# Optimization experiments

Measured on AMD Instinct MI355X. Metric: run time of the kernel, lower is better.

The kernel has to match this reference:

```python
import jax, jax.numpy as jnp
import numpy as np


def setup_inputs() -> dict:
    key = jax.random.key(0)
    ks = jax.random.split(key, 6)
    B, F, C = 2048, 512, 64
    t_feat = jax.random.normal(ks[0], (B, F), dtype=jnp.float32)
    f_feat = jax.random.normal(ks[1], (B, F), dtype=jnp.float32)
    # proj Linear(F*F -> C); scale like torch default init (~1/sqrt(fan_in))
    W_proj = jax.random.normal(ks[2], (C, F * F), dtype=jnp.float32) / np.sqrt(F * F)
    b_proj = jnp.zeros((C,), dtype=jnp.float32)
    W1 = jax.random.normal(ks[3], (32, C), dtype=jnp.float32) / np.sqrt(C)
    b1 = jnp.zeros((32,), dtype=jnp.float32)
    W2 = jax.random.normal(ks[4], (1, 32), dtype=jnp.float32) / np.sqrt(32)
    b2 = jnp.zeros((1,), dtype=jnp.float32)
    return {"t_feat": t_feat, "f_feat": f_feat, "W_proj": W_proj, "b_proj": b_proj,
            "W1": W1, "b1": b1, "W2": W2, "b2": b2}


def reference(t_feat, f_feat, W_proj, b_proj, W1, b1, W2, b2):
    B, F = t_feat.shape
    C = W_proj.shape[0]
    # corr[b,i,j] = t[b,i] * f[b,j]; proj = corr_flat @ W_proj.T + b_proj.
    # Equivalent bilinear form computed WITHOUT materializing the (B,F,F) outer product:
    Wr = W_proj.reshape(C, F, F)            # W_proj[c, i*F + j] -> Wr[c,i,j]
    tmp = jnp.einsum('bi,cij->bcj', t_feat, Wr)   # (B, C, F)
    proj = jnp.einsum('bcj,bj->bc', tmp, f_feat) + b_proj  # (B, C)
    h = jax.nn.relu(proj)
    # GRL is identity in forward
    h2 = jax.nn.relu(h @ W1.T + b1)          # (B, 32)
    logit = h2 @ W2.T + b2                   # (B, 1)
    return logit
```

## Files before the change

kernel.cpp:

```cpp
#include <hip/hip_runtime.h>
#include <hip/hip_bf16.h>
#include <stdint.h>

#define BATCH 2048
#define FDIM 512
#define CDIM 64

typedef unsigned short ushort_t;
typedef __attribute__((ext_vector_type(8))) short short8;
typedef __attribute__((ext_vector_type(4))) float f32x4;

__device__ __forceinline__ ushort_t f2bf(float x) {
    union { float f; uint32_t u; } v; v.f = x;
    uint32_t u = v.u;
    uint32_t r = u + 0x7FFFu + ((u >> 16) & 1u);
    return (ushort_t)(r >> 16);
}
__device__ __forceinline__ float bf2f(ushort_t u) {
    union { float f; uint32_t v; } x; x.v = ((uint32_t)u) << 16; return x.f;
}

__global__ void convert_kernel(const float* __restrict__ src, ushort_t* __restrict__ dst) {
    int idx = blockIdx.x * 256 + threadIdx.x;
    float4 v0 = ((const float4*)src)[idx * 2];
    float4 v1 = ((const float4*)src)[idx * 2 + 1];
    ushort_t p[8] = { f2bf(v0.x), f2bf(v0.y), f2bf(v0.z), f2bf(v0.w),
                      f2bf(v1.x), f2bf(v1.y), f2bf(v1.z), f2bf(v1.w) };
    *(uint4*)&dst[idx * 8] = *(uint4*)p;
}

__global__ void convert_ft_kernel(const float* __restrict__ f, ushort_t* __restrict__ f16,
                                  const float* __restrict__ t, ushort_t* __restrict__ t16) {
    int blk = blockIdx.x;
    const float* src = (blk < 512) ? f : t;
    ushort_t* dst    = (blk < 512) ? f16 : t16;
    int idx = (blk & 511) * 256 + threadIdx.x;
    float4 v0 = ((const float4*)src)[idx * 2];
    float4 v1 = ((const float4*)src)[idx * 2 + 1];
    ushort_t p[8] = { f2bf(v0.x), f2bf(v0.y), f2bf(v0.z), f2bf(v0.w),
                      f2bf(v1.x), f2bf(v1.y), f2bf(v1.z), f2bf(v1.w) };
    *(uint4*)&dst[idx * 8] = *(uint4*)p;
}

#define AS3(p) ((__attribute__((address_space(3))) void*)(p))
#define AS1(p) ((const __attribute__((address_space(1))) void*)(p))

__launch_bounds__(256, 2)
__global__ void gemm_fused_kernel(const ushort_t* __restrict__ f16,
                                  const ushort_t* __restrict__ Wb,
                                  const ushort_t* __restrict__ t16,
                                  float* __restrict__ part) {
    __shared__ ushort_t As[128 * 32];
    __shared__ ushort_t Bs[128 * 32];
    __shared__ float scratch[256];

    const int tid  = threadIdx.x;
    const int wave = tid >> 6;
    const int lane = tid & 63;
    const int l15  = lane & 15;
    const int lg   = lane >> 4;

    const int b0 = blockIdx.x * 128;
    const int n0 = blockIdx.y * 128;

    const int m_base = (wave >> 1) * 64;
    const int nh     = wave & 1;
    const int n_base = nh * 64;

    f32x4 acc[4][4];
    #pragma unroll
    for (int mi = 0; mi < 4; mi++)
        #pragma unroll
        for (int ni = 0; ni < 4; ni++)
            acc[mi][ni] = (f32x4){0.f, 0.f, 0.f, 0.f};

    const int p    = tid >> 2;
    const int cph  = tid & 3;
    const int cg   = cph ^ ((p >> 1) & 3);
    const int nrot = ((p & 15) << 2) | (p >> 4);

    const ushort_t* gA0 = f16 + (size_t)(b0 + p) * FDIM + cg * 8;
    const ushort_t* gA1 = f16 + (size_t)(b0 + 64 + p) * FDIM + cg * 8;
    const ushort_t* gB0 = Wb + (size_t)(n0 + nrot) * FDIM + cg * 8;
    const ushort_t* gB1 = Wb + (size_t)(n0 + 64 + nrot) * FDIM + cg * 8;

    for (int k0 = 0; k0 < FDIM; k0 += 32) {
        __builtin_amdgcn_global_load_lds(AS1(gA0 + k0), AS3(&As[0 * 2048 + wave * 512]), 16, 0, 0);
        __builtin_amdgcn_global_load_lds(AS1(gA1 + k0), AS3(&As[1 * 2048 + wave * 512]), 16, 0, 0);
        __builtin_amdgcn_global_load_lds(AS1(gB0 + k0), AS3(&Bs[0 * 2048 + wave * 512]), 16, 0, 0);
        __builtin_amdgcn_global_load_lds(AS1(gB1 + k0), AS3(&Bs[1 * 2048 + wave * 512]), 16, 0, 0);
        __syncthreads();

        short8 a[4], b[4];
        #pragma unroll
        for (int mi = 0; mi < 4; mi++) {
            int r = m_base + mi * 16 + l15;
            a[mi] = *(const short8*)&As[r * 32 + (lg ^ ((r >> 1) & 3)) * 8];
        }
        #pragma unroll
        for (int ni = 0; ni < 4; ni++) {
            int q = n_base + ni * 16 + l15;
            b[ni] = *(const short8*)&Bs[q * 32 + (lg ^ ((q >> 1) & 3)) * 8];
        }

        #pragma unroll
        for (int mi = 0; mi < 4; mi++)
            #pragma unroll
            for (int ni = 0; ni < 4; ni++)
                acc[mi][ni] = __builtin_amdgcn_mfma_f32_16x16x32_bf16(a[mi], b[ni], acc[mi][ni], 0, 0, 0);

        __syncthreads();
    }

    const int c  = n0 >> 9;
    const int iq = (n0 >> 7) & 3;
    const int i_base = (n0 & 511) + n_base + l15 * 4;

    #pragma unroll
    for (int mi = 0; mi < 4; mi++) {
        #pragma unroll
        for (int r = 0; r < 4; r++) {
            int b_idx = b0 + m_base + mi * 16 + lg * 4 + r;
            ushort4 tv = *(const ushort4*)&t16[(size_t)b_idx * FDIM + i_base];
            float sv = acc[mi][0][r] * bf2f(tv.x) + acc[mi][1][r] * bf2f(tv.y)
                     + acc[mi][2][r] * bf2f(tv.z) + acc[mi][3][r] * bf2f(tv.w);
            sv += __shfl_xor(sv, 1, 64);
            sv += __shfl_xor(sv, 2, 64);
            sv += __shfl_xor(sv, 4, 64);
            sv += __shfl_xor(sv, 8, 64);
            if (l15 == 0)
                scratch[(m_base + mi * 16 + lg * 4 + r) * 2 + nh] = sv;
        }
    }
    __syncthreads();
    if (tid < 128) {
        float v = scratch[tid * 2] + scratch[tid * 2 + 1];
        part[(((size_t)(b0 + tid)) * 64 + c) * 4 + iq] = v;
    }
}

__global__ void mlp_kernel(const float* __restrict__ part,
                           const float* __restrict__ b_proj,
                           const float* __restrict__ W1, const float* __restrict__ b1,
                           const float* __restrict__ W2, const float* __restrict__ b2,
                           float* __restrict__ out) {
    __shared__ float h[8][64];
    const int tid = threadIdx.x;
    const int bl  = tid >> 5;
    const int o   = tid & 31;
    const int b   = blockIdx.x * 8 + bl;

    #pragma unroll
    for (int c = o; c < 64; c += 32) {
        float4 v = *(const float4*)&part[(((size_t)b * 64 + c)) * 4];
        float sv = v.x + v.y + v.z + v.w + b_proj[c];
        h[bl][c] = sv > 0.f ? sv : 0.f;
    }
    __syncthreads();

    float sv = b1[o];
    #pragma unroll
    for (int c = 0; c < 64; c++) sv += h[bl][c] * W1[o * 64 + c];
    float v = (sv > 0.f ? sv : 0.f) * W2[o];
    v += __shfl_xor(v, 1, 32);
    v += __shfl_xor(v, 2, 32);
    v += __shfl_xor(v, 4, 32);
    v += __shfl_xor(v, 8, 32);
    v += __shfl_xor(v, 16, 32);
    if (o == 0) out[b] = v + b2[0];
}

extern "C" void kernel_launch(void* const* d_in, const int* in_sizes, int n_in,
                              void* d_out, int out_size, void* d_ws, size_t ws_size,
                              hipStream_t stream) {
    const float* t_feat = (const float*)d_in[0];
    const float* f_feat = (const float*)d_in[1];
    const float* W_proj = (const float*)d_in[2];
    const float* b_proj = (const float*)d_in[3];
    const float* W1     = (const float*)d_in[4];
    const float* b1     = (const float*)d_in[5];
    const float* W2     = (const float*)d_in[6];
    const float* b2     = (const float*)d_in[7];
    float* out = (float*)d_out;

    uint8_t* ws = (uint8_t*)d_ws;
    ushort_t* Wb   = (ushort_t*)(ws);
    ushort_t* f16  = (ushort_t*)(ws + 33554432);
    ushort_t* t16  = (ushort_t*)(ws + 33554432 + 2097152);
    float*    part = (float*)(ws + 33554432 + 2 * 2097152);

    convert_kernel<<<dim3((CDIM * FDIM * FDIM) / 2048), dim3(256), 0, stream>>>(W_proj, Wb);
    convert_ft_kernel<<<dim3(1024), dim3(256), 0, stream>>>(f_feat, f16, t_feat, t16);

    gemm_fused_kernel<<<dim3(BATCH / 128, (CDIM * FDIM) / 128), dim3(256), 0, stream>>>(
        f16, Wb, t16, part);

    mlp_kernel<<<dim3(BATCH / 8), dim3(256), 0, stream>>>(part, b_proj, W1, b1, W2, b2, out);
}
```

Measured before the change: 213.9 us.

## Merge conversion kernels and fuse MLP tail into GEMM via last-block counter

The three bf16 conversion passes are merged into one prep kernel, which also zeroes a per-row-tile atomic counter. The separate MLP kernel is folded into the GEMM: each block increments a counter after writing its partials, and the last of the 256 column blocks for a row tile runs the bias, ReLU and two small linear layers for those 128 rows. This removes two kernel launches and their gaps. In exchange it adds threadfences and atomics, and the tail is serialised onto one block per row tile, with a per-thread 64-element array that may raise register pressure.

```diff
diff --git a/kernel.cpp b/kernel.cpp
--- a/kernel.cpp
+++ b/kernel.cpp
@@ -20,8 +20,19 @@
     union { float f; uint32_t v; } x; x.v = ((uint32_t)u) << 16; return x.f;
 }
 
-__global__ void convert_kernel(const float* __restrict__ src, ushort_t* __restrict__ dst) {
-    int idx = blockIdx.x * 256 + threadIdx.x;
+#define WCH ((CDIM * FDIM * FDIM) / 8)
+#define FCH ((BATCH * FDIM) / 8)
+
+__global__ void prep_kernel(const float* __restrict__ W, ushort_t* __restrict__ Wb,
+                            const float* __restrict__ f, ushort_t* __restrict__ f16,
+                            const float* __restrict__ t, ushort_t* __restrict__ t16,
+                            unsigned int* __restrict__ cnt) {
+    if (blockIdx.x == 0 && threadIdx.x < 16) cnt[threadIdx.x] = 0;
+    int gid = blockIdx.x * 256 + threadIdx.x;
+    const float* src; ushort_t* dst; int idx;
+    if (gid < WCH)            { src = W; dst = Wb;  idx = gid; }
+    else if (gid < WCH + FCH) { src = f; dst = f16; idx = gid - WCH; }
+    else                      { src = t; dst = t16; idx = gid - WCH - FCH; }
     float4 v0 = ((const float4*)src)[idx * 2];
     float4 v1 = ((const float4*)src)[idx * 2 + 1];
     ushort_t p[8] = { f2bf(v0.x), f2bf(v0.y), f2bf(v0.z), f2bf(v0.w),
@@ -29,19 +40,6 @@
     *(uint4*)&dst[idx * 8] = *(uint4*)p;
 }
 
-__global__ void convert_ft_kernel(const float* __restrict__ f, ushort_t* __restrict__ f16,
-                                  const float* __restrict__ t, ushort_t* __restrict__ t16) {
-    int blk = blockIdx.x;
-    const float* src = (blk < 512) ? f : t;
-    ushort_t* dst    = (blk < 512) ? f16 : t16;
-    int idx = (blk & 511) * 256 + threadIdx.x;
-    float4 v0 = ((const float4*)src)[idx * 2];
-    float4 v1 = ((const float4*)src)[idx * 2 + 1];
-    ushort_t p[8] = { f2bf(v0.x), f2bf(v0.y), f2bf(v0.z), f2bf(v0.w),
-                      f2bf(v1.x), f2bf(v1.y), f2bf(v1.z), f2bf(v1.w) };
-    *(uint4*)&dst[idx * 8] = *(uint4*)p;
-}
-
 #define AS3(p) ((__attribute__((address_space(3))) void*)(p))
 #define AS1(p) ((const __attribute__((address_space(1))) void*)(p))
 
@@ -49,10 +47,18 @@
 __global__ void gemm_fused_kernel(const ushort_t* __restrict__ f16,
                                   const ushort_t* __restrict__ Wb,
                                   const ushort_t* __restrict__ t16,
-                                  float* __restrict__ part) {
+                                  float* __restrict__ part,
+                                  unsigned int* __restrict__ cnt,
+                                  const float* __restrict__ b_proj,
+                                  const float* __restrict__ W1,
+                                  const float* __restrict__ b1,
+                                  const float* __restrict__ W2,
+                                  const float* __restrict__ b2,
+                                  float* __restrict__ out) {
     __shared__ ushort_t As[128 * 32];
     __shared__ ushort_t Bs[128 * 32];
     __shared__ float scratch[256];
+    __shared__ int is_last;
 
     const int tid  = threadIdx.x;
     const int wave = tid >> 6;
@@ -137,37 +143,35 @@
         float v = scratch[tid * 2] + scratch[tid * 2 + 1];
         part[(((size_t)(b0 + tid)) * 64 + c) * 4 + iq] = v;
     }
-}
-
-__global__ void mlp_kernel(const float* __restrict__ part,
-                           const float* __restrict__ b_proj,
-                           const float* __restrict__ W1, const float* __restrict__ b1,
-                           const float* __restrict__ W2, const float* __restrict__ b2,
-                           float* __restrict__ out) {
-    __shared__ float h[8][64];
-    const int tid = threadIdx.x;
-    const int bl  = tid >> 5;
-    const int o   = tid & 31;
-    const int b   = blockIdx.x * 8 + bl;
-
-    #pragma unroll
-    for (int c = o; c < 64; c += 32) {
-        float4 v = *(const float4*)&part[(((size_t)b * 64 + c)) * 4];
-        float sv = v.x + v.y + v.z + v.w + b_proj[c];
-        h[bl][c] = sv > 0.f ? sv : 0.f;
+
+    __threadfence();
+    if (tid == 0) {
+        unsigned int old = atomicAdd(&cnt[blockIdx.x], 1u);
+        is_last = (old == 255u);
     }
     __syncthreads();
-
-    float sv = b1[o];
-    #pragma unroll
-    for (int c = 0; c < 64; c++) sv += h[bl][c] * W1[o * 64 + c];
-    float v = (sv > 0.f ? sv : 0.f) * W2[o];
-    v += __shfl_xor(v, 1, 32);
-    v += __shfl_xor(v, 2, 32);
-    v += __shfl_xor(v, 4, 32);
-    v += __shfl_xor(v, 8, 32);
-    v += __shfl_xor(v, 16, 32);
-    if (o == 0) out[b] = v + b2[0];
+    if (is_last) {
+        __threadfence();
+        if (tid < 128) {
+            int row = b0 + tid;
+            const float4* p4 = (const float4*)&part[(size_t)row * 256];
+            float h[64];
+            #pragma unroll
+            for (int cc = 0; cc < 64; cc++) {
+                float4 v = p4[cc];
+                float sv = v.x + v.y + v.z + v.w + b_proj[cc];
+                h[cc] = sv > 0.f ? sv : 0.f;
+            }
+            float logit = b2[0];
+            for (int o = 0; o < 32; o++) {
+                float sv = b1[o];
+                #pragma unroll
+                for (int cc = 0; cc < 64; cc++) sv += h[cc] * W1[o * 64 + cc];
+                logit += (sv > 0.f ? sv : 0.f) * W2[o];
+            }
+            out[row] = logit;
+        }
+    }
 }
 
 extern "C" void kernel_launch(void* const* d_in, const int* in_sizes, int n_in,
@@ -186,14 +190,13 @@
     uint8_t* ws = (uint8_t*)d_ws;
     ushort_t* Wb   = (ushort_t*)(ws);
     ushort_t* f16  = (ushort_t*)(ws + 33554432);
-    ushort_t* t16  = (ushort_t*)(ws + 33554432 + 2097152);
-    float*    part = (float*)(ws + 33554432 + 2 * 2097152);
-
-    convert_kernel<<<dim3((CDIM * FDIM * FDIM) / 2048), dim3(256), 0, stream>>>(W_proj, Wb);
-    convert_ft_kernel<<<dim3(1024), dim3(256), 0, stream>>>(f_feat, f16, t_feat, t16);
+    ushort_t* t16  = (ushort_t*)(ws + 35651584);
+    float*    part = (float*)(ws + 37748736);
+    unsigned int* cnt = (unsigned int*)(ws + 39845888);
+
+    prep_kernel<<<dim3(WCH / 256 + (2 * FCH) / 256), dim3(256), 0, stream>>>(
+        W_proj, Wb, f_feat, f16, t_feat, t16, cnt);
 
     gemm_fused_kernel<<<dim3(BATCH / 128, (CDIM * FDIM) / 128), dim3(256), 0, stream>>>(
-        f16, Wb, t16, part);
-
-    mlp_kernel<<<dim3(BATCH / 8), dim3(256), 0, stream>>>(part, b_proj, W1, b1, W2, b2, out);
-}
+        f16, Wb, t16, part, cnt, b_proj, W1, b1, W2, b2, out);
+}
```

Result: slower. 673.7 us (+214.9%).

## Fuse W_proj bf16 conversion into GEMM B loads, drop separate convert pass

Applied to the files above, without the earlier changes.

Drops the standalone kernel that converted the 64x512x512 fp32 W_proj to bf16 in workspace. The GEMM now loads fp32 W rows straight into registers and converts them to bf16 in-kernel, without LDS staging for B. Blocks use a 1D grid that groups the 16 batch tiles sharing one W tile onto adjacent block ids, and launch bounds rise to 4 blocks per CU. This avoids writing and re-reading a 32MB intermediate, but W is now fetched as fp32 and reconverted by each of the 16 batch blocks, relying on L2 to absorb the reuse.

```diff
diff --git a/kernel.cpp b/kernel.cpp
--- a/kernel.cpp
+++ b/kernel.cpp
@@ -20,21 +20,14 @@
     union { float f; uint32_t v; } x; x.v = ((uint32_t)u) << 16; return x.f;
 }
 
-__global__ void convert_kernel(const float* __restrict__ src, ushort_t* __restrict__ dst) {
-    int idx = blockIdx.x * 256 + threadIdx.x;
-    float4 v0 = ((const float4*)src)[idx * 2];
-    float4 v1 = ((const float4*)src)[idx * 2 + 1];
-    ushort_t p[8] = { f2bf(v0.x), f2bf(v0.y), f2bf(v0.z), f2bf(v0.w),
-                      f2bf(v1.x), f2bf(v1.y), f2bf(v1.z), f2bf(v1.w) };
-    *(uint4*)&dst[idx * 8] = *(uint4*)p;
-}
+#define FCH ((BATCH * FDIM) / 8)
 
-__global__ void convert_ft_kernel(const float* __restrict__ f, ushort_t* __restrict__ f16,
-                                  const float* __restrict__ t, ushort_t* __restrict__ t16) {
-    int blk = blockIdx.x;
-    const float* src = (blk < 512) ? f : t;
-    ushort_t* dst    = (blk < 512) ? f16 : t16;
-    int idx = (blk & 511) * 256 + threadIdx.x;
+__global__ void prep_kernel(const float* __restrict__ f, ushort_t* __restrict__ f16,
+                            const float* __restrict__ t, ushort_t* __restrict__ t16) {
+    int gid = blockIdx.x * 256 + threadIdx.x;
+    const float* src = (gid < FCH) ? f : t;
+    ushort_t* dst    = (gid < FCH) ? f16 : t16;
+    int idx = gid & (FCH - 1);
     float4 v0 = ((const float4*)src)[idx * 2];
     float4 v1 = ((const float4*)src)[idx * 2 + 1];
     ushort_t p[8] = { f2bf(v0.x), f2bf(v0.y), f2bf(v0.z), f2bf(v0.w),
@@ -45,13 +38,12 @@
 #define AS3(p) ((__attribute__((address_space(3))) void*)(p))
 #define AS1(p) ((const __attribute__((address_space(1))) void*)(p))
 
-__launch_bounds__(256, 2)
+__launch_bounds__(256, 4)
 __global__ void gemm_fused_kernel(const ushort_t* __restrict__ f16,
-                                  const ushort_t* __restrict__ Wb,
+                                  const float* __restrict__ W,
                                   const ushort_t* __restrict__ t16,
                                   float* __restrict__ part) {
     __shared__ ushort_t As[128 * 32];
-    __shared__ ushort_t Bs[128 * 32];
     __shared__ float scratch[256];
 
     const int tid  = threadIdx.x;
@@ -60,8 +52,10 @@
     const int l15  = lane & 15;
     const int lg   = lane >> 4;
 
-    const int b0 = blockIdx.x * 128;
-    const int n0 = blockIdx.y * 128;
+    const int g  = blockIdx.x;
+    const int s  = g >> 3;
+    const int b0 = (s & 15) << 7;
+    const int n0 = (((g & 7) << 5) + (s >> 4)) << 7;
 
     const int m_base = (wave >> 1) * 64;
     const int nh     = wave & 1;
@@ -74,33 +68,38 @@
         for (int ni = 0; ni < 4; ni++)
             acc[mi][ni] = (f32x4){0.f, 0.f, 0.f, 0.f};
 
-    const int p    = tid >> 2;
-    const int cph  = tid & 3;
-    const int cg   = cph ^ ((p >> 1) & 3);
-    const int nrot = ((p & 15) << 2) | (p >> 4);
-
+    const int p   = tid >> 2;
+    const int cph = tid & 3;
+    const int cg  = cph ^ ((p >> 1) & 3);
     const ushort_t* gA0 = f16 + (size_t)(b0 + p) * FDIM + cg * 8;
     const ushort_t* gA1 = f16 + (size_t)(b0 + 64 + p) * FDIM + cg * 8;
-    const ushort_t* gB0 = Wb + (size_t)(n0 + nrot) * FDIM + cg * 8;
-    const ushort_t* gB1 = Wb + (size_t)(n0 + 64 + nrot) * FDIM + cg * 8;
+
+    const float* gB = W + (size_t)(n0 + n_base + l15 * 4) * FDIM + lg * 8;
 
     for (int k0 = 0; k0 < FDIM; k0 += 32) {
+        short8 b[4];
+        #pragma unroll
+        for (int ni = 0; ni < 4; ni++) {
+            const float* bp = gB + (size_t)ni * FDIM + k0;
+            float4 v0 = *(const float4*)bp;
+            float4 v1 = *(const float4*)(bp + 4);
+            union { __hip_bfloat162 h2[4]; short8 s8; } pk;
+            pk.h2[0] = __float22bfloat162_rn(make_float2(v0.x, v0.y));
+            pk.h2[1] = __float22bfloat162_rn(make_float2(v0.z, v0.w));
+            pk.h2[2] = __float22bfloat162_rn(make_float2(v1.x, v1.y));
+            pk.h2[3] = __float22bfloat162_rn(make_float2(v1.z, v1.w));
+            b[ni] = pk.s8;
+        }
+
         __builtin_amdgcn_global_load_lds(AS1(gA0 + k0), AS3(&As[0 * 2048 + wave * 512]), 16, 0, 0);
         __builtin_amdgcn_global_load_lds(AS1(gA1 + k0), AS3(&As[1 * 2048 + wave * 512]), 16, 0, 0);
-        __builtin_amdgcn_global_load_lds(AS1(gB0 + k0), AS3(&Bs[0 * 2048 + wave * 512]), 16, 0, 0);
-        __builtin_amdgcn_global_load_lds(AS1(gB1 + k0), AS3(&Bs[1 * 2048 + wave * 512]), 16, 0, 0);
         __syncthreads();
 
-        short8 a[4], b[4];
+        short8 a[4];
         #pragma unroll
         for (int mi = 0; mi < 4; mi++) {
             int r = m_base + mi * 16 + l15;
             a[mi] = *(const short8*)&As[r * 32 + (lg ^ ((r >> 1) & 3)) * 8];
-        }
-        #pragma unroll
-        for (int ni = 0; ni < 4; ni++) {
-            int q = n_base + ni * 16 + l15;
-            b[ni] = *(const short8*)&Bs[q * 32 + (lg ^ ((q >> 1) & 3)) * 8];
         }
 
         #pragma unroll
@@ -184,16 +183,13 @@
     float* out = (float*)d_out;
 
     uint8_t* ws = (uint8_t*)d_ws;
-    ushort_t* Wb   = (ushort_t*)(ws);
-    ushort_t* f16  = (ushort_t*)(ws + 33554432);
-    ushort_t* t16  = (ushort_t*)(ws + 33554432 + 2097152);
-    float*    part = (float*)(ws + 33554432 + 2 * 2097152);
+    ushort_t* f16  = (ushort_t*)(ws);
+    ushort_t* t16  = (ushort_t*)(ws + 2097152);
+    float*    part = (float*)(ws + 4194304);
 
-    convert_kernel<<<dim3((CDIM * FDIM * FDIM) / 2048), dim3(256), 0, stream>>>(W_proj, Wb);
-    convert_ft_kernel<<<dim3(1024), dim3(256), 0, stream>>>(f_feat, f16, t_feat, t16);
+    prep_kernel<<<dim3((2 * FCH) / 256), dim3(256), 0, stream>>>(f_feat, f16, t_feat, t16);
 
-    gemm_fused_kernel<<<dim3(BATCH / 128, (CDIM * FDIM) / 128), dim3(256), 0, stream>>>(
-        f16, Wb, t16, part);
+    gemm_fused_kernel<<<dim3(4096), dim3(256), 0, stream>>>(f16, W_proj, t16, part);
 
     mlp_kernel<<<dim3(BATCH / 8), dim3(256), 0, stream>>>(part, b_proj, W1, b1, W2, b2, out);
 }
```

Measured after the change: 364.7 us. +70.5%, slower.
